# Kernel optimization log

Measured on AMD Instinct MI355X. Metric: run time of the kernel, lower is better.

The kernel has to match this reference:

```python
import jax, jax.numpy as jnp
import numpy as np

B, S, H, NH, L, ML = 4, 2048, 768, 8, 128, 15
DH = H // NH
PERIOD = 16  # newline every 16 tokens -> 15 content tokens per line


def _layernorm(x, g, b, eps=1e-5):
    m = x.mean(-1, keepdims=True)
    v = ((x - m) ** 2).mean(-1, keepdims=True)
    return (x - m) / jnp.sqrt(v + eps) * g + b


def setup_inputs() -> dict:
    key = jax.random.key(0)
    ks = jax.random.split(key, 8)
    sc = 0.02
    return {
        "hidden": jax.random.normal(ks[0], (B, S, H), jnp.float32),
        "in_proj_w": jax.random.normal(ks[1], (3 * H, H), jnp.float32) * sc,
        "in_proj_b": jnp.zeros((3 * H,), jnp.float32),
        "out_proj_w": jax.random.normal(ks[2], (H, H), jnp.float32) * sc,
        "out_proj_b": jnp.zeros((H,), jnp.float32),
        "W1": jax.random.normal(ks[3], (H, 2 * H), jnp.float32) * sc,
        "b1": jnp.zeros((H,), jnp.float32),
        "g1": jnp.ones((H,), jnp.float32),
        "be1": jnp.zeros((H,), jnp.float32),
        "W2": jax.random.normal(ks[4], (H, H), jnp.float32) * sc,
        "b2": jnp.zeros((H,), jnp.float32),
        "g2": jnp.ones((H,), jnp.float32),
        "be2": jnp.zeros((H,), jnp.float32),
        "W3": jax.random.normal(ks[5], (1, H), jnp.float32) * sc,
        "b3": jnp.zeros((1,), jnp.float32),
        # padded ragged line structure (what the torch loops derive from newline positions)
        "line_starts": jnp.tile(jnp.arange(L, dtype=jnp.int32) * PERIOD, (B, 1)),  # [B,L]
        "line_lens": jnp.full((B, L), ML, jnp.int32),                              # [B,L]
        "context_len": jnp.full((B,), S, jnp.int32),                               # [B]
    }


def reference(hidden, in_proj_w, in_proj_b, out_proj_w, out_proj_b,
              W1, b1, g1, be1, W2, b2, g2, be2, W3, b3,
              line_starts, line_lens, context_len):
    # --- gather per-line tokens into a padded [B, L, ML, H] block ---
    pos = line_starts[:, :, None] + jnp.arange(ML, dtype=line_starts.dtype)      # [B,L,ML]
    tok_mask = jnp.arange(ML)[None, None, :] < line_lens[:, :, None]             # [B,L,ML]
    pos_c = jnp.clip(pos, 0, S - 1)
    bidx = jnp.arange(B)[:, None, None]
    line_tok = hidden[bidx, pos_c]                                               # [B,L,ML,H]

    # --- nn.MultiheadAttention: query=line tokens, key/value=global context ---
    Wq, Wk, Wv = jnp.split(in_proj_w, 3, axis=0)
    bq, bk, bv = jnp.split(in_proj_b, 3, axis=0)
    q = (line_tok @ Wq.T + bq).reshape(B, L, ML, NH, DH)
    k = (hidden @ Wk.T + bk).reshape(B, S, NH, DH)
    v = (hidden @ Wv.T + bv).reshape(B, S, NH, DH)

    scale = 1.0 / np.float32(np.sqrt(DH))
    scores = jnp.einsum('blmhd,bshd->blhms', q, k) * scale                       # [B,L,NH,ML,S]
    kmask = jnp.arange(S)[None, :] < context_len[:, None]                        # [B,S]
    scores = jnp.where(kmask[:, None, None, None, :], scores, -1e9)
    attn = jax.nn.softmax(scores, axis=-1)
    o = jnp.einsum('blhms,bshd->blmhd', attn, v).reshape(B, L, ML, H)
    o = o @ out_proj_w.T + out_proj_b                                            # [B,L,ML,H]

    # --- masked mean-pool over the line's tokens ---
    m = tok_mask[..., None].astype(hidden.dtype)
    denom = jnp.maximum(line_lens, 1)[..., None].astype(hidden.dtype)            # [B,L,1]
    line_mean = (line_tok * m).sum(2) / denom                                    # [B,L,H]
    attn_mean = (o * m).sum(2) / denom                                           # [B,L,H]

    # --- classifier: Linear -> LN -> GELU -> Residual(Linear->LN->GELU) -> Linear ---
    x = jnp.concatenate([line_mean, attn_mean], axis=-1)                         # [B,L,2H]
    x = jax.nn.gelu(_layernorm(x @ W1.T + b1, g1, be1), approximate=False)
    x = x + jax.nn.gelu(_layernorm(x @ W2.T + b2, g2, be2), approximate=False)
    logits = (x @ W3.T + b3)[..., 0]                                             # [B,L]

    # empty lines get logit -10 (as in the torch loop)
    logits = jnp.where(line_lens > 0, logits, jnp.asarray(-10.0, logits.dtype))
    return jax.nn.sigmoid(logits)
```

## Files before the change

kernel.cpp:

```cpp
#include <hip/hip_runtime.h>
#include <hip/hip_bf16.h>
#include <cmath>

using bf16 = __hip_bfloat16;
typedef __attribute__((ext_vector_type(8))) short short8;
typedef __attribute__((ext_vector_type(4))) short s16x4;
typedef __attribute__((ext_vector_type(4))) float f32x4;

#define B_   4
#define S_   2048
#define H_   768
#define H2_  1536
#define H3_  2304
#define NH_  8
#define DH_  96
#define L_   128
#define ML_  15
#define LG_  8
#define QR_  128
#define CH_  32
#define NS_  2
#define SLC_ (S_ / NS_)
#define ELD  36
#define VTLD 36
#define VTR  112

__device__ __forceinline__ float gelu_exact(float v) {
    return 0.5f * v * (1.0f + erff(v * 0.7071067811865475f));
}
__device__ __forceinline__ short f2bs(float f) {
    bf16 h = __float2bfloat16(f);
    return *reinterpret_cast<short*>(&h);
}
__device__ __forceinline__ short8 ld_frag8(const short* p) {
    union { short8 v; s16x4 h[2]; } u;
    u.h[0] = *(const s16x4*)p;
    u.h[1] = *(const s16x4*)(p + 4);
    return u.v;
}

__global__ __launch_bounds__(256) void f2b_k(
    const float* __restrict__ src, bf16* __restrict__ dst, int n)
{
    const int i = (blockIdx.x * 256 + threadIdx.x) * 8;
    if (i >= n) return;
    float4 a = *(const float4*)(src + i);
    float4 b = *(const float4*)(src + i + 4);
    short8 r;
    r[0] = f2bs(a.x); r[1] = f2bs(a.y); r[2] = f2bs(a.z); r[3] = f2bs(a.w);
    r[4] = f2bs(b.x); r[5] = f2bs(b.y); r[6] = f2bs(b.z); r[7] = f2bs(b.w);
    *(short8*)(dst + i) = r;
}

template <typename T>
__device__ __forceinline__ void stage8(const T* src, bf16* dst);
template <>
__device__ __forceinline__ void stage8<bf16>(const bf16* src, bf16* dst) {
    *(int4*)dst = *(const int4*)src;
}
template <>
__device__ __forceinline__ void stage8<float>(const float* src, bf16* dst) {
    float4 a = *(const float4*)src;
    float4 b = *(const float4*)(src + 4);
    short8 r;
    r[0] = f2bs(a.x); r[1] = f2bs(a.y); r[2] = f2bs(a.z); r[3] = f2bs(a.w);
    r[4] = f2bs(b.x); r[5] = f2bs(b.y); r[6] = f2bs(b.z); r[7] = f2bs(b.w);
    *(short8*)dst = r;
}

__global__ __launch_bounds__(256) void gemm128_bt(
    const bf16* __restrict__ A, const bf16* __restrict__ Bm,
    const float* __restrict__ bias, bf16* __restrict__ C,
    int M, int N, int K, int ldc)
{
    __shared__ alignas(16) bf16 As[128 * 32];
    __shared__ alignas(16) bf16 Bs[128 * 32];
    const int t = threadIdx.x;
    const int wave = t >> 6, lane = t & 63;
    const int l15 = lane & 15, quad = lane >> 4;
    const int m0 = blockIdx.x * 128, n0 = blockIdx.y * 128;
    const int wm = wave & 1, wn = wave >> 1;
    const int srow = t >> 1, scol = (t & 1) * 16;

    const bf16* aP = A + (size_t)(m0 + srow) * K + scol;
    const bf16* bP = Bm + (size_t)(n0 + srow) * K + scol;
    bf16* aL = &As[srow * 32 + scol];
    bf16* bL = &Bs[srow * 32 + scol];

    f32x4 acc[4][4];
#pragma unroll
    for (int i = 0; i < 4; i++)
#pragma unroll
        for (int j = 0; j < 4; j++) acc[i][j] = (f32x4){0.f, 0.f, 0.f, 0.f};

    for (int k0 = 0; k0 < K; k0 += 32) {
        int4 ra0 = *(const int4*)(aP + k0);
        int4 ra1 = *(const int4*)(aP + k0 + 8);
        int4 rb0 = *(const int4*)(bP + k0);
        int4 rb1 = *(const int4*)(bP + k0 + 8);
        __syncthreads();
        *(int4*)aL = ra0; *(int4*)(aL + 8) = ra1;
        *(int4*)bL = rb0; *(int4*)(bL + 8) = rb1;
        __syncthreads();
        short8 af[4], bfq[4];
#pragma unroll
        for (int i = 0; i < 4; i++)
            af[i] = *(const short8*)&As[(wm * 64 + i * 16 + l15) * 32 + quad * 8];
#pragma unroll
        for (int j = 0; j < 4; j++)
            bfq[j] = *(const short8*)&Bs[(wn * 64 + j * 16 + l15) * 32 + quad * 8];
#pragma unroll
        for (int i = 0; i < 4; i++)
#pragma unroll
            for (int j = 0; j < 4; j++)
                acc[i][j] = __builtin_amdgcn_mfma_f32_16x16x32_bf16(af[i], bfq[j], acc[i][j], 0, 0, 0);
    }

#pragma unroll
    for (int j = 0; j < 4; j++) {
        const int col = n0 + wn * 64 + j * 16 + l15;
        const float bv = bias[col];
#pragma unroll
        for (int i = 0; i < 4; i++) {
            const int row = m0 + wm * 64 + i * 16 + quad * 4;
#pragma unroll
            for (int r = 0; r < 4; r++)
                C[(size_t)(row + r) * ldc + col] = __float2bfloat16(acc[i][j][r] + bv);
        }
    }
}

template <typename TA, typename TB, bool OUT_BF16>
__global__ __launch_bounds__(256) void gemm_bt(
    const TA* __restrict__ A, const TB* __restrict__ Bm,
    const float* __restrict__ bias, void* __restrict__ Cout,
    int M, int N, int K, int ldc, int coff)
{
    __shared__ alignas(16) bf16 As[64 * 32];
    __shared__ alignas(16) bf16 Bs[64 * 32];
    const int t = threadIdx.x;
    const int wave = t >> 6, lane = t & 63;
    const int l15 = lane & 15, quad = lane >> 4;
    const int m0 = blockIdx.x * 64, n0 = blockIdx.y * 64;
    const int srow = t >> 2, schk = (t & 3) * 8;

    const TA* aPtr = A + (size_t)(m0 + srow) * K + schk;
    const TB* bPtr = Bm + (size_t)(n0 + srow) * K + schk;

    f32x4 acc[4] = {{0.f,0.f,0.f,0.f},{0.f,0.f,0.f,0.f},
                    {0.f,0.f,0.f,0.f},{0.f,0.f,0.f,0.f}};
    const int aoff = (wave * 16 + l15) * 32 + quad * 8;

    for (int k0 = 0; k0 < K; k0 += 32) {
        __syncthreads();
        stage8<TA>(aPtr + k0, &As[srow * 32 + schk]);
        stage8<TB>(bPtr + k0, &Bs[srow * 32 + schk]);
        __syncthreads();
        short8 af = *(const short8*)&As[aoff];
#pragma unroll
        for (int nt = 0; nt < 4; nt++) {
            short8 bfr = *(const short8*)&Bs[(nt * 16 + l15) * 32 + quad * 8];
            acc[nt] = __builtin_amdgcn_mfma_f32_16x16x32_bf16(af, bfr, acc[nt], 0, 0, 0);
        }
    }

#pragma unroll
    for (int nt = 0; nt < 4; nt++) {
        int col = n0 + nt * 16 + l15;
        float bv = bias[col];
#pragma unroll
        for (int r = 0; r < 4; r++) {
            int row = m0 + wave * 16 + quad * 4 + r;
            float v = acc[nt][r] + bv;
            if (OUT_BF16) ((bf16*)Cout)[(size_t)row * ldc + coff + col] = __float2bfloat16(v);
            else          ((float*)Cout)[(size_t)row * ldc + coff + col] = v;
        }
    }
}

__global__ __launch_bounds__(256) void attn_slice(
    const bf16* __restrict__ qkv, const int* __restrict__ line_starts,
    const int* __restrict__ line_lens, const int* __restrict__ context_len,
    bf16* __restrict__ Opart, float* __restrict__ Dpart)
{
    __shared__ alignas(16) union {
        short Qs[QR_ * DH_];
        struct {
            short Ks[CH_ * DH_];
            short Vt[VTR * VTLD];
            short Es[QR_ * ELD];
        } s;
    } U;

    const int t = threadIdx.x;
    const int idx = blockIdx.x;
    const int slice = blockIdx.y;
    const int lg = idx & 15;
    const int bh = idx >> 4;
    const int h = bh & 7, b = bh >> 3;
    const int ctx = context_len[b];
    const int wave = t >> 6, lane = t & 63;
    const int l15 = lane & 15, quad = lane >> 4;

    for (int ii = t; ii < QR_ * 12; ii += 256) {
        const int r = ii / 12, ck = ii - r * 12;
        int4 val; val.x = val.y = val.z = val.w = 0;
        if (r < LG_ * ML_) {
            const int li = r / ML_, m = r - li * ML_;
            const int line = lg * LG_ + li;
            const int len = line_lens[b * L_ + line];
            if (m < len) {
                int sPos = line_starts[b * L_ + line] + m;
                sPos = min(max(sPos, 0), S_ - 1);
                val = *(const int4*)(qkv + (size_t)(b * S_ + sPos) * H3_ + h * DH_ + ck * 8);
            }
        }
        ((int4*)U.Qs)[ii] = val;
    }
    __syncthreads();

    short8 qf[2][3];
#pragma unroll
    for (int st = 0; st < 2; st++)
#pragma unroll
        for (int kf = 0; kf < 3; kf++)
            qf[st][kf] = *(const short8*)(U.Qs + ((wave + 4 * st) * 16 + l15) * DH_ + kf * 32 + quad * 8);
    __syncthreads();

    f32x4 Oacc[2][7];
#pragma unroll
    for (int st = 0; st < 2; st++)
#pragma unroll
        for (int nt = 0; nt < 7; nt++) Oacc[st][nt] = (f32x4){0.f, 0.f, 0.f, 0.f};

    const float scale = 0.10206207261596577f;
    const size_t kbase = (size_t)b * S_ * H3_ + H_ + h * DH_;
    const size_t vbase = kbase + H_;
    const int cbase = slice * SLC_;

    const int vt_qp = t / 12;
    const int vt_ck = t - vt_qp * 12;
    const int on_dd = t >> 4;
    const int on_sp = t & 15;

    int4 rk0, rk1; short8 rva, rvb;
    const int ki0 = 2 * t, ki1 = 2 * t + 1;
    if (t < 192) {
        rk0 = *(const int4*)(qkv + kbase + (size_t)(cbase + ki0 / 12) * H3_ + (ki0 % 12) * 8);
        rk1 = *(const int4*)(qkv + kbase + (size_t)(cbase + ki1 / 12) * H3_ + (ki1 % 12) * 8);
        const bf16* vs = qkv + vbase + (size_t)(cbase + 2 * vt_qp) * H3_ + vt_ck * 8;
        rva = *(const short8*)vs;
        rvb = *(const short8*)(vs + H3_);
    }

    for (int ci = 0; ci < SLC_ / CH_; ci++) {
        const int c0 = cbase + ci * CH_;
        __syncthreads();
        if (t < 192) {
            ((int4*)U.s.Ks)[ki0] = rk0;
            ((int4*)U.s.Ks)[ki1] = rk1;
#pragma unroll
            for (int j = 0; j < 8; j++) {
                unsigned int pk = (unsigned int)(unsigned short)rva[j]
                                | ((unsigned int)(unsigned short)rvb[j] << 16);
                *(unsigned int*)&U.s.Vt[(vt_ck * 8 + j) * VTLD + 2 * vt_qp] = pk;
            }
        }
        {
            unsigned int lo = (c0 + 2 * on_sp)     < ctx ? 0x3f80u : 0u;
            unsigned int hi = (c0 + 2 * on_sp + 1) < ctx ? 0x3f80u : 0u;
            *(unsigned int*)&U.s.Vt[(96 + on_dd) * VTLD + 2 * on_sp] = lo | (hi << 16);
        }
        __syncthreads();

        if (ci + 1 < SLC_ / CH_ && t < 192) {
            const int cn = c0 + CH_;
            rk0 = *(const int4*)(qkv + kbase + (size_t)(cn + ki0 / 12) * H3_ + (ki0 % 12) * 8);
            rk1 = *(const int4*)(qkv + kbase + (size_t)(cn + ki1 / 12) * H3_ + (ki1 % 12) * 8);
            const bf16* vs = qkv + vbase + (size_t)(cn + 2 * vt_qp) * H3_ + vt_ck * 8;
            rva = *(const short8*)vs;
            rvb = *(const short8*)(vs + H3_);
        }

        f32x4 acc[2][2] = {{{0.f,0.f,0.f,0.f},{0.f,0.f,0.f,0.f}},
                           {{0.f,0.f,0.f,0.f},{0.f,0.f,0.f,0.f}}};
#pragma unroll
        for (int nt = 0; nt < 2; nt++)
#pragma unroll
            for (int kf = 0; kf < 3; kf++) {
                short8 kfr = *(const short8*)(U.s.Ks + (nt * 16 + l15) * DH_ + kf * 32 + quad * 8);
                acc[0][nt] = __builtin_amdgcn_mfma_f32_16x16x32_bf16(qf[0][kf], kfr, acc[0][nt], 0, 0, 0);
                acc[1][nt] = __builtin_amdgcn_mfma_f32_16x16x32_bf16(qf[1][kf], kfr, acc[1][nt], 0, 0, 0);
            }

#pragma unroll
        for (int st = 0; st < 2; st++)
#pragma unroll
            for (int nt = 0; nt < 2; nt++) {
                const int c = nt * 16 + l15;
                const bool kok = (c0 + c) < ctx;
#pragma unroll
                for (int r = 0; r < 4; r++) {
                    float e = kok ? __expf(acc[st][nt][r] * scale) : 0.f;
                    U.s.Es[((wave + 4 * st) * 16 + quad * 4 + r) * ELD + c] = f2bs(e);
                }
            }

        short8 pf0 = ld_frag8(U.s.Es + (wave * 16 + l15) * ELD + quad * 8);
        short8 pf1 = ld_frag8(U.s.Es + ((wave + 4) * 16 + l15) * ELD + quad * 8);
#pragma unroll
        for (int nt = 0; nt < 7; nt++) {
            short8 vfr = ld_frag8(U.s.Vt + (nt * 16 + l15) * VTLD + quad * 8);
            Oacc[0][nt] = __builtin_amdgcn_mfma_f32_16x16x32_bf16(pf0, vfr, Oacc[0][nt], 0, 0, 0);
            Oacc[1][nt] = __builtin_amdgcn_mfma_f32_16x16x32_bf16(pf1, vfr, Oacc[1][nt], 0, 0, 0);
        }
    }

    const size_t pb = (size_t)(slice * 512 + idx) * QR_;
#pragma unroll
    for (int st = 0; st < 2; st++)
#pragma unroll
        for (int r = 0; r < 4; r++) {
            const int row = (wave + 4 * st) * 16 + quad * 4 + r;
#pragma unroll
            for (int nt = 0; nt < 6; nt++)
                Opart[(pb + row) * DH_ + nt * 16 + l15] = __float2bfloat16(Oacc[st][nt][r]);
            if (l15 == 0) Dpart[pb + row] = Oacc[st][6][r];
        }
}

__global__ __launch_bounds__(256) void combine_pool(
    const bf16* __restrict__ Opart, const float* __restrict__ Dpart,
    const int* __restrict__ line_lens, bf16* __restrict__ opool)
{
    __shared__ float invd[LG_ * ML_];
    __shared__ int lens_s[LG_];
    const int idx = blockIdx.x;
    const int lg = idx & 15, bh = idx >> 4;
    const int h = bh & 7, b = bh >> 3;
    const int t = threadIdx.x;
    if (t < LG_) lens_s[t] = line_lens[b * L_ + lg * LG_ + t];
    if (t < LG_ * ML_) {
        float ds = 0.f;
#pragma unroll
        for (int s = 0; s < NS_; s++)
            ds += Dpart[(size_t)(s * 512 + idx) * QR_ + t];
        invd[t] = ds > 0.f ? 1.f / ds : 0.f;
    }
    __syncthreads();
    for (int q = t; q < LG_ * DH_; q += 256) {
        const int li = q / DH_, d = q - li * DH_;
        const int mm = min(lens_s[li], ML_);
        float acc = 0.f;
        for (int m = 0; m < mm; m++) {
            const int row = li * ML_ + m;
            float o = 0.f;
#pragma unroll
            for (int s = 0; s < NS_; s++)
                o += __bfloat162float(Opart[((size_t)(s * 512 + idx) * QR_ + row) * DH_ + d]);
            acc += o * invd[row];
        }
        const int line = lg * LG_ + li;
        opool[(size_t)(b * L_ + line) * H_ + h * DH_ + d] =
            __float2bfloat16(acc / (float)max(lens_s[li], 1));
    }
}

__global__ __launch_bounds__(256) void line_mean_k(
    const bf16* __restrict__ hidden, const int* __restrict__ line_starts,
    const int* __restrict__ line_lens, bf16* __restrict__ x)
{
    const int blk = blockIdx.x;
    const int b = blk >> 7, line = blk & 127;
    const int len = line_lens[b * L_ + line];
    const int start = line_starts[b * L_ + line];
    const int mm = min(len, ML_);
    const float inv = 1.f / (float)max(len, 1);
    for (int d = threadIdx.x; d < H_; d += 256) {
        float s = 0.f;
        for (int m = 0; m < mm; m++) {
            int sp = min(max(start + m, 0), S_ - 1);
            s += __bfloat162float(hidden[(size_t)(b * S_ + sp) * H_ + d]);
        }
        x[(size_t)blk * H2_ + d] = __float2bfloat16(s * inv);
    }
}

__global__ __launch_bounds__(256) void ln_gelu_k(
    const float* __restrict__ hin, const float* __restrict__ g,
    const float* __restrict__ be, float* __restrict__ uout, bf16* __restrict__ ubf)
{
    __shared__ float red[16];
    const int row = blockIdx.x, t = threadIdx.x;
    const float* hr = hin + (size_t)row * H_;
    float v[3];
    float s1 = 0.f, s2 = 0.f;
#pragma unroll
    for (int k = 0; k < 3; k++) {
        v[k] = hr[t + k * 256];
        s1 += v[k]; s2 += v[k] * v[k];
    }
#pragma unroll
    for (int m = 1; m < 64; m <<= 1) { s1 += __shfl_xor(s1, m, 64); s2 += __shfl_xor(s2, m, 64); }
    const int wave = t >> 6, lane = t & 63;
    if (lane == 0) { red[wave] = s1; red[8 + wave] = s2; }
    __syncthreads();
    s1 = red[0] + red[1] + red[2] + red[3];
    s2 = red[8] + red[9] + red[10] + red[11];
    const float mean = s1 * (1.f / H_);
    const float var = s2 * (1.f / H_) - mean * mean;
    const float rstd = 1.f / sqrtf(var + 1e-5f);
#pragma unroll
    for (int k = 0; k < 3; k++) {
        const int d = t + k * 256;
        float y = (v[k] - mean) * rstd * g[d] + be[d];
        y = gelu_exact(y);
        uout[(size_t)row * H_ + d] = y;
        ubf[(size_t)row * H_ + d] = __float2bfloat16(y);
    }
}

__global__ __launch_bounds__(256) void final_k(
    const float* __restrict__ h2, const float* __restrict__ u,
    const float* __restrict__ g2, const float* __restrict__ be2,
    const float* __restrict__ W3, const float* __restrict__ b3,
    const int* __restrict__ line_lens, float* __restrict__ out)
{
    __shared__ float red[16];
    const int row = blockIdx.x, t = threadIdx.x;
    const float* hr = h2 + (size_t)row * H_;
    float v[3];
    float s1 = 0.f, s2 = 0.f;
#pragma unroll
    for (int k = 0; k < 3; k++) {
        v[k] = hr[t + k * 256];
        s1 += v[k]; s2 += v[k] * v[k];
    }
#pragma unroll
    for (int m = 1; m < 64; m <<= 1) { s1 += __shfl_xor(s1, m, 64); s2 += __shfl_xor(s2, m, 64); }
    const int wave = t >> 6, lane = t & 63;
    if (lane == 0) { red[wave] = s1; red[8 + wave] = s2; }
    __syncthreads();
    s1 = red[0] + red[1] + red[2] + red[3];
    s2 = red[8] + red[9] + red[10] + red[11];
    const float mean = s1 * (1.f / H_);
    const float var = s2 * (1.f / H_) - mean * mean;
    const float rstd = 1.f / sqrtf(var + 1e-5f);
    float dotp = 0.f;
#pragma unroll
    for (int k = 0; k < 3; k++) {
        const int d = t + k * 256;
        float y = (v[k] - mean) * rstd * g2[d] + be2[d];
        y = u[(size_t)row * H_ + d] + gelu_exact(y);
        dotp += y * W3[d];
    }
#pragma unroll
    for (int m = 1; m < 64; m <<= 1) dotp += __shfl_xor(dotp, m, 64);
    __syncthreads();
    if (lane == 0) red[wave] = dotp;
    __syncthreads();
    if (t == 0) {
        float logit = red[0] + red[1] + red[2] + red[3] + b3[0];
        if (line_lens[row] <= 0) logit = -10.f;
        out[row] = 1.f / (1.f + __expf(-logit));
    }
}

extern "C" void kernel_launch(void* const* d_in, const int* in_sizes, int n_in,
                              void* d_out, int out_size, void* d_ws, size_t ws_size,
                              hipStream_t stream)
{
    const float* hidden     = (const float*)d_in[0];
    const float* in_proj_w  = (const float*)d_in[1];
    const float* in_proj_b  = (const float*)d_in[2];
    const float* out_proj_w = (const float*)d_in[3];
    const float* out_proj_b = (const float*)d_in[4];
    const float* W1         = (const float*)d_in[5];
    const float* b1         = (const float*)d_in[6];
    const float* g1         = (const float*)d_in[7];
    const float* be1        = (const float*)d_in[8];
    const float* W2         = (const float*)d_in[9];
    const float* b2         = (const float*)d_in[10];
    const float* g2         = (const float*)d_in[11];
    const float* be2        = (const float*)d_in[12];
    const float* W3         = (const float*)d_in[13];
    const float* b3         = (const float*)d_in[14];
    const int* line_starts  = (const int*)d_in[15];
    const int* line_lens    = (const int*)d_in[16];
    const int* context_len  = (const int*)d_in[17];

    const int BL = B_ * L_;
    const size_t nh = (size_t)B_ * S_ * H_;
    const size_t nw = (size_t)H3_ * H_;
    const size_t opart_n = (size_t)NS_ * 512 * QR_ * DH_;

    char* w = (char*)d_ws;
    bf16* qkv   = (bf16*)w;  w += (size_t)B_ * S_ * H3_ * sizeof(bf16);
    char* ovl = w;
    bf16* hb    = (bf16*)ovl;
    bf16* wqkvb = (bf16*)(ovl + nh * sizeof(bf16));
    bf16* Opart = (bf16*)ovl;
    w = ovl + opart_n * sizeof(bf16);
    float* Dpart = (float*)w; w += (size_t)NS_ * 512 * QR_ * sizeof(float);
    bf16* opool = (bf16*)w;  w += (size_t)BL * H_ * sizeof(bf16);
    bf16* x     = (bf16*)w;  w += (size_t)BL * H2_ * sizeof(bf16);
    float* h1   = (float*)w; w += (size_t)BL * H_ * sizeof(float);
    float* uu   = (float*)w; w += (size_t)BL * H_ * sizeof(float);
    bf16* ubf   = (bf16*)w;  w += (size_t)BL * H_ * sizeof(bf16);
    float* h2   = (float*)w; w += (size_t)BL * H_ * sizeof(float);

    f2b_k<<<(int)(nh / (256 * 8)), 256, 0, stream>>>(hidden, hb, (int)nh);
    f2b_k<<<(int)(nw / (256 * 8)), 256, 0, stream>>>(in_proj_w, wqkvb, (int)nw);

    gemm128_bt<<<dim3(B_ * S_ / 128, H3_ / 128), 256, 0, stream>>>(
        hb, wqkvb, in_proj_b, qkv, B_ * S_, H3_, H_, H3_);
    line_mean_k<<<BL, 256, 0, stream>>>(hb, line_starts, line_lens, x);
    attn_slice<<<dim3(512, NS_), 256, 0, stream>>>(
        qkv, line_starts, line_lens, context_len, Opart, Dpart);
    combine_pool<<<512, 256, 0, stream>>>(Opart, Dpart, line_lens, opool);
    gemm_bt<bf16, float, true><<<dim3(BL / 64, H_ / 64), 256, 0, stream>>>(
        opool, out_proj_w, out_proj_b, x, BL, H_, H_, H2_, H_);
    gemm_bt<bf16, float, false><<<dim3(BL / 64, H_ / 64), 256, 0, stream>>>(
        x, W1, b1, h1, BL, H_, H2_, H_, 0);
    ln_gelu_k<<<BL, 256, 0, stream>>>(h1, g1, be1, uu, ubf);
    gemm_bt<bf16, float, false><<<dim3(BL / 64, H_ / 64), 256, 0, stream>>>(
        ubf, W2, b2, h2, BL, H_, H_, H_, 0);
    final_k<<<BL, 256, 0, stream>>>(h2, uu, g2, be2, W3, b3, line_lens, (float*)d_out);
}
```

Baseline: 376.8 us.

## Pad attention LDS tiles and transpose score MFMA for vectorized P writes

Pads the Q/K shared-memory rows to 104 and the V-transpose rows to 56 to reduce LDS bank conflicts. The MFMA operands in QK^T are swapped, so each lane holds four consecutive key positions for one query row. The exp results can then be packed and written to the P tile as one 4-short vector store instead of four scalar stores. V fragments are now read with a single 16-byte load, which the new 56-short row stride keeps 16-byte aligned. The cost is more LDS per block, which could reduce occupancy.

```diff
diff --git a/kernel.cpp b/kernel.cpp
--- a/kernel.cpp
+++ b/kernel.cpp
@@ -22,7 +22,8 @@
 #define NS_  2
 #define SLC_ (S_ / NS_)
 #define ELD  36
-#define VTLD 36
+#define VTLD 56
+#define KLD  104
 #define VTR  112
 
 __device__ __forceinline__ float gelu_exact(float v) {
@@ -184,9 +185,9 @@
     bf16* __restrict__ Opart, float* __restrict__ Dpart)
 {
     __shared__ alignas(16) union {
-        short Qs[QR_ * DH_];
+        short Qs[QR_ * KLD];
         struct {
-            short Ks[CH_ * DH_];
+            short Ks[CH_ * KLD];
             short Vt[VTR * VTLD];
             short Es[QR_ * ELD];
         } s;
@@ -215,7 +216,7 @@
                 val = *(const int4*)(qkv + (size_t)(b * S_ + sPos) * H3_ + h * DH_ + ck * 8);
             }
         }
-        ((int4*)U.Qs)[ii] = val;
+        *(int4*)&U.Qs[r * KLD + ck * 8] = val;
     }
     __syncthreads();
 
@@ -224,7 +225,7 @@
     for (int st = 0; st < 2; st++)
 #pragma unroll
         for (int kf = 0; kf < 3; kf++)
-            qf[st][kf] = *(const short8*)(U.Qs + ((wave + 4 * st) * 16 + l15) * DH_ + kf * 32 + quad * 8);
+            qf[st][kf] = *(const short8*)(U.Qs + ((wave + 4 * st) * 16 + l15) * KLD + kf * 32 + quad * 8);
     __syncthreads();
 
     f32x4 Oacc[2][7];
@@ -257,8 +258,8 @@
         const int c0 = cbase + ci * CH_;
         __syncthreads();
         if (t < 192) {
-            ((int4*)U.s.Ks)[ki0] = rk0;
-            ((int4*)U.s.Ks)[ki1] = rk1;
+            *(int4*)&U.s.Ks[(ki0 / 12) * KLD + (ki0 % 12) * 8] = rk0;
+            *(int4*)&U.s.Ks[(ki1 / 12) * KLD + (ki1 % 12) * 8] = rk1;
 #pragma unroll
             for (int j = 0; j < 8; j++) {
                 unsigned int pk = (unsigned int)(unsigned short)rva[j]
@@ -285,32 +286,33 @@
         f32x4 acc[2][2] = {{{0.f,0.f,0.f,0.f},{0.f,0.f,0.f,0.f}},
                            {{0.f,0.f,0.f,0.f},{0.f,0.f,0.f,0.f}}};
 #pragma unroll
-        for (int nt = 0; nt < 2; nt++)
+        for (int ns = 0; ns < 2; ns++)
 #pragma unroll
             for (int kf = 0; kf < 3; kf++) {
-                short8 kfr = *(const short8*)(U.s.Ks + (nt * 16 + l15) * DH_ + kf * 32 + quad * 8);
-                acc[0][nt] = __builtin_amdgcn_mfma_f32_16x16x32_bf16(qf[0][kf], kfr, acc[0][nt], 0, 0, 0);
-                acc[1][nt] = __builtin_amdgcn_mfma_f32_16x16x32_bf16(qf[1][kf], kfr, acc[1][nt], 0, 0, 0);
+                short8 kfr = *(const short8*)(U.s.Ks + (ns * 16 + l15) * KLD + kf * 32 + quad * 8);
+                acc[0][ns] = __builtin_amdgcn_mfma_f32_16x16x32_bf16(kfr, qf[0][kf], acc[0][ns], 0, 0, 0);
+                acc[1][ns] = __builtin_amdgcn_mfma_f32_16x16x32_bf16(kfr, qf[1][kf], acc[1][ns], 0, 0, 0);
             }
 
 #pragma unroll
         for (int st = 0; st < 2; st++)
 #pragma unroll
-            for (int nt = 0; nt < 2; nt++) {
-                const int c = nt * 16 + l15;
-                const bool kok = (c0 + c) < ctx;
+            for (int ns = 0; ns < 2; ns++) {
+                s16x4 wv;
 #pragma unroll
                 for (int r = 0; r < 4; r++) {
-                    float e = kok ? __expf(acc[st][nt][r] * scale) : 0.f;
-                    U.s.Es[((wave + 4 * st) * 16 + quad * 4 + r) * ELD + c] = f2bs(e);
+                    const int s = c0 + ns * 16 + quad * 4 + r;
+                    float e = (s < ctx) ? __expf(acc[st][ns][r] * scale) : 0.f;
+                    wv[r] = f2bs(e);
                 }
+                *(s16x4*)&U.s.Es[((wave + 4 * st) * 16 + l15) * ELD + ns * 16 + quad * 4] = wv;
             }
 
         short8 pf0 = ld_frag8(U.s.Es + (wave * 16 + l15) * ELD + quad * 8);
         short8 pf1 = ld_frag8(U.s.Es + ((wave + 4) * 16 + l15) * ELD + quad * 8);
 #pragma unroll
         for (int nt = 0; nt < 7; nt++) {
-            short8 vfr = ld_frag8(U.s.Vt + (nt * 16 + l15) * VTLD + quad * 8);
+            short8 vfr = *(const short8*)&U.s.Vt[(nt * 16 + l15) * VTLD + quad * 8];
             Oacc[0][nt] = __builtin_amdgcn_mfma_f32_16x16x32_bf16(pf0, vfr, Oacc[0][nt], 0, 0, 0);
             Oacc[1][nt] = __builtin_amdgcn_mfma_f32_16x16x32_bf16(pf1, vfr, Oacc[1][nt], 0, 0, 0);
         }
```

Result: no change. 370.7 us (-1.6%).
